# Kernel optimization log

Measured on AMD Instinct MI355X. Metric: run time of the kernel, lower is better.

## Reference

```python
import jax, jax.numpy as jnp
import numpy as np

B, DIM, L = 16, 512, 4096          # batch, hidden, num frames
N_FFT, HOP, WIN = 1024, 256, 1024  # STFT config (padding='same')


def setup_inputs() -> dict:
    key = jax.random.key(0)
    k1, k2, k3 = jax.random.split(key, 3)
    x = jax.random.normal(k1, (B, DIM, L), dtype=jnp.float32)
    # Conv1d(dim, 2*n_fft, kernel_size=1) weight/bias; small scale so exp(mag) stays sane
    W = jax.random.normal(k2, (2 * N_FFT, DIM), dtype=jnp.float32) * 0.02
    b = jax.random.normal(k3, (2 * N_FFT,), dtype=jnp.float32) * 0.02
    return {"x": x, "W": W, "b": b}


def reference(x, W, b):
    # 1x1 conv == channel-mixing GEMM: (B, 2*n_fft, L)
    h = jnp.einsum('bdl,od->bol', x, W) + b[None, :, None]
    mag, p = jnp.split(h, 2, axis=1)            # each (B, n_fft, L)
    mag = jnp.minimum(jnp.exp(mag), 100.0)      # exp then clip(max=100)
    S = mag * jax.lax.complex(jnp.cos(p), jnp.sin(p))
    # torch.fft.irfft(S, n_fft, dim=1): crops freq axis to n_fft//2+1 bins
    frames = jnp.fft.irfft(S, n=N_FFT, axis=1)
    # hann window, periodic=True (torch default)
    window = 0.5 * (1.0 - jnp.cos(2.0 * jnp.pi * jnp.arange(WIN, dtype=jnp.float32) / WIN))
    frames = frames * window[None, :, None]
    T = frames.shape[-1]
    out_len = (T - 1) * HOP + WIN
    idx = jnp.arange(T)[None, :] * HOP + jnp.arange(WIN)[:, None]
    y = jnp.zeros((frames.shape[0], out_len), frames.dtype).at[:, idx].add(frames)
    env = jnp.zeros((out_len,), frames.dtype).at[idx].add(
        jnp.broadcast_to((window * window)[:, None], (WIN, T)))
    pad = (WIN - HOP) // 2                      # 'same' padding trim
    return y[:, pad:out_len - pad] / env[pad:out_len - pad]
```

## Files before the change

### kernel.cpp

```cpp
#include <hip/hip_runtime.h>
#include <cstdint>
#include <cstddef>

#define BATCH  16
#define DIMK   512
#define LEN    4096
#define NFFT   1024
#define HOPS   256
#define PADT   384
#define OUTL   1048576
#define KP2    1056
#define KP2U   528
#define K2     4224

typedef __attribute__((ext_vector_type(8))) short  short8;
typedef __attribute__((ext_vector_type(4))) float  f32x4;

__device__ __forceinline__ unsigned short f2bf(float f) {
    unsigned u = __float_as_uint(f);
    u += 0x7FFFu + ((u >> 16) & 1u);
    return (unsigned short)(u >> 16);
}

__device__ __forceinline__ void gld16(const unsigned short* g, unsigned short* l) {
    __builtin_amdgcn_global_load_lds(
        (const __attribute__((address_space(1))) unsigned int*)(const void*)g,
        (__attribute__((address_space(3))) unsigned int*)(void*)l, 16, 0, 0);
}

__global__ void pack_W(const float* __restrict__ W, const float* __restrict__ bvec,
                       unsigned short* __restrict__ Wb, float* __restrict__ bp) {
    const int r = blockIdx.x;
    const int i = r >> 7, j = r & 127;
    const int src = (j < 64) ? (i * 64 + j) : (1024 + i * 64 + (j - 64));
    for (int c = threadIdx.x; c < DIMK; c += 256)
        Wb[r * DIMK + c] = f2bf(W[src * DIMK + c]);
    if (threadIdx.x == 0) bp[r] = bvec[src];
}

__global__ void transpose_x(const float* __restrict__ x, unsigned short* __restrict__ xT) {
    __shared__ float tile[32][33];
    const int b = blockIdx.z;
    const int l0 = blockIdx.x * 32, d0 = blockIdx.y * 32;
    const int tx = threadIdx.x, ty = threadIdx.y;
#pragma unroll
    for (int i = 0; i < 4; ++i)
        tile[ty + 8 * i][tx] = x[((size_t)b * DIMK + d0 + ty + 8 * i) * LEN + l0 + tx];
    __syncthreads();
#pragma unroll
    for (int i = 0; i < 4; ++i)
        xT[((size_t)b * LEN + l0 + ty + 8 * i) * DIMK + d0 + tx] = f2bf(tile[tx][ty + 8 * i]);
}

__global__ void build_D(unsigned short* __restrict__ D) {
    const int idx = blockIdx.x * 256 + threadIdx.x;
    if (idx >= 256 * K2) return;
    const int srow = idx / K2;
    const int col  = idx - srow * K2;
    const int rseg = col / KP2;
    const int jj   = col - rseg * KP2;
    const int n    = srow + 256 * rseg;
    const int k    = jj >> 1;
    const float wv = 0.5f - 0.5f * __cosf((float)n * (6.283185307179586f / 1024.f));
    float v = 0.f;
    if ((jj & 1) == 0) {
        if (k == 0)        v = wv * (1.f / 1024.f);
        else if (k < 512) {
            const int p = (k * n) & 1023;
            v = 2.f * __cosf((float)p * (6.283185307179586f / 1024.f)) * wv * (1.f / 1024.f);
        } else if (k == 512) v = ((n & 1) ? -wv : wv) * (1.f / 1024.f);
    } else {
        if (k >= 1 && k < 512) {
            const int p = (k * n) & 1023;
            v = -2.f * __sinf((float)p * (6.283185307179586f / 1024.f)) * wv * (1.f / 1024.f);
        }
    }
    D[idx] = f2bf(v);
}

__global__ __launch_bounds__(256)
void gemm1_kernel(const unsigned short* __restrict__ A,
                  const unsigned short* __restrict__ Bm,
                  const float* __restrict__ bp,
                  unsigned* __restrict__ Sout)
{
    __shared__ alignas(16) char smem[17408];
    unsigned short* Alds = (unsigned short*)smem;
    unsigned short* Blds = (unsigned short*)(smem + 8192);
    unsigned*       epi  = (unsigned*)smem;

    const int tid  = threadIdx.x;
    const int lane = tid & 63, w = tid >> 6;
    const int quad = lane >> 4, ln = lane & 15;
    const int bx = blockIdx.x, by = blockIdx.y, bz = blockIdx.z;
    const int l0 = bx * 128;

    const int c0 = tid, c1 = tid + 256;
    const unsigned short* Bsrc0 = Bm + ((size_t)bz * LEN + l0 + (c0 >> 2)) * DIMK + (c0 & 3) * 8;
    const unsigned short* Bsrc1 = Bm + ((size_t)bz * LEN + l0 + (c1 >> 2)) * DIMK + (c1 & 3) * 8;

    for (int mi = 0; mi < 3; ++mi) {
        const int mt = by * 3 + mi;
        const int m0 = mt * 128;
        const int kbase = mt * 64;

        const unsigned short* Asrc0 = A + (size_t)(m0 + (c0 >> 2)) * DIMK + (c0 & 3) * 8;
        const unsigned short* Asrc1 = A + (size_t)(m0 + (c1 >> 2)) * DIMK + (c1 & 3) * 8;

        f32x4 acc[8][2];
#pragma unroll
        for (int a = 0; a < 8; ++a)
#pragma unroll
            for (int c = 0; c < 2; ++c) acc[a][c] = (f32x4){0.f, 0.f, 0.f, 0.f};

        for (int k0 = 0; k0 < DIMK; k0 += 32) {
            gld16(Asrc0 + k0, &Alds[c0 * 8]);
            gld16(Asrc1 + k0, &Alds[c1 * 8]);
            gld16(Bsrc0 + k0, &Blds[c0 * 8]);
            gld16(Bsrc1 + k0, &Blds[c1 * 8]);
            __syncthreads();

            short8 af[8], bfr[2];
#pragma unroll
            for (int rt = 0; rt < 8; ++rt)
                af[rt] = *(const short8*)&Alds[((16 * rt + ln) * 4 + quad) * 8];
#pragma unroll
            for (int ct = 0; ct < 2; ++ct)
                bfr[ct] = *(const short8*)&Blds[((32 * w + 16 * ct + ln) * 4 + quad) * 8];
#pragma unroll
            for (int rt = 0; rt < 8; ++rt)
#pragma unroll
                for (int ct = 0; ct < 2; ++ct)
                    acc[rt][ct] = __builtin_amdgcn_mfma_f32_16x16x32_bf16(af[rt], bfr[ct], acc[rt][ct], 0, 0, 0);
            __syncthreads();
        }

#pragma unroll
        for (int ct = 0; ct < 2; ++ct) {
            const int lrow = w * 16 + ln;
#pragma unroll
            for (int rt = 0; rt < 4; ++rt) {
                unsigned pk[4];
#pragma unroll
                for (int reg = 0; reg < 4; ++reg) {
                    const int rloc = 16 * rt + quad * 4 + reg;
                    const float hm = acc[rt][ct][reg]     + bp[m0 + rloc];
                    const float hp = acc[rt + 4][ct][reg] + bp[m0 + 64 + rloc];
                    const float mag = fminf(__expf(hm), 100.0f);
                    pk[reg] = (unsigned)f2bf(mag * __cosf(hp)) |
                              ((unsigned)f2bf(mag * __sinf(hp)) << 16);
                }
                *(uint4*)&epi[lrow * 68 + 16 * rt + 4 * quad] = *(uint4*)pk;
            }
            __syncthreads();
#pragma unroll
            for (int i = 0; i < 4; ++i) {
                const int c = i * 256 + tid;
                const int row = c >> 4, kc = c & 15;
                if (kbase + kc * 4 < KP2U) {
                    const int l = l0 + 32 * (row >> 4) + 16 * ct + (row & 15);
                    uint4 v = *(const uint4*)&epi[row * 68 + kc * 4];
                    *(uint4*)&Sout[((size_t)bz * LEN + l) * KP2U + kbase + kc * 4] = v;
                }
            }
            __syncthreads();
        }
    }
}

__device__ __forceinline__ float env_at(int q, int s) {
    float env = 0.f;
#pragma unroll
    for (int r = 0; r < 4; ++r) {
        const int t = q - r;
        if (t >= 0 && t < LEN) {
            const float w = 0.5f - 0.5f * __cosf((float)(s + 256 * r) * (6.283185307179586f / 1024.f));
            env += w * w;
        }
    }
    return env;
}

__global__ __launch_bounds__(256)
void gemm2_kernel(const unsigned short* __restrict__ D,
                  const unsigned short* __restrict__ Sm,
                  float* __restrict__ yout)
{
    __shared__ alignas(16) char smem[24832];
    unsigned short* Albuf = (unsigned short*)smem;
    unsigned short* Blds  = (unsigned short*)(smem + 16384);
    float*          epi   = (float*)smem;

    const int tid  = threadIdx.x;
    const int lane = tid & 63, w = tid >> 6;
    const int quad = lane >> 4, ln = lane & 15;
    const int sh = w >> 1, qh = w & 1;
    const int bx = blockIdx.x, by = blockIdx.y, bz = blockIdx.z;
    const int qt0 = bx * 128, s0 = by * 128;

    const size_t srowbase = (size_t)bz * LEN;
    const int ca0 = tid, ca1 = tid + 256;

    f32x4 acc[4][4];
#pragma unroll
    for (int a = 0; a < 4; ++a)
#pragma unroll
        for (int c = 0; c < 4; ++c) acc[a][c] = (f32x4){0.f, 0.f, 0.f, 0.f};

    for (int kk = 0; kk < KP2; kk += 32) {
        {
            const int r0 = ca0 >> 2, q0 = ca0 & 3, le0 = qt0 + r0 - 2;
            const int r1 = ca1 >> 2, q1 = ca1 & 3, le1 = qt0 + r1 - 2;
            uint4 v0 = {0, 0, 0, 0}, v1 = {0, 0, 0, 0};
            if ((unsigned)le0 < (unsigned)LEN)
                v0 = *(const uint4*)&Sm[(srowbase + le0) * KP2 + kk + q0 * 8];
            if ((unsigned)le1 < (unsigned)LEN)
                v1 = *(const uint4*)&Sm[(srowbase + le1) * KP2 + kk + q1 * 8];
            *(uint4*)&Blds[ca0 * 8] = v0;
            *(uint4*)&Blds[ca1 * 8] = v1;
            if (tid < 16) {
                const int c2 = 512 + tid;
                const int r2 = c2 >> 2, q2 = c2 & 3, le2 = qt0 + r2 - 2;
                uint4 v2 = {0, 0, 0, 0};
                if ((unsigned)le2 < (unsigned)LEN)
                    v2 = *(const uint4*)&Sm[(srowbase + le2) * KP2 + kk + q2 * 8];
                *(uint4*)&Blds[c2 * 8] = v2;
            }
        }
        gld16(D + (size_t)(s0 + (ca0 >> 2)) * K2 + kk + (ca0 & 3) * 8, &Albuf[ca0 * 8]);
        gld16(D + (size_t)(s0 + (ca1 >> 2)) * K2 + kk + (ca1 & 3) * 8, &Albuf[ca1 * 8]);
        __syncthreads();

#pragma unroll
        for (int rseg = 0; rseg < 4; ++rseg) {
            const int buf = rseg & 1;
            if (rseg < 3) {
                const unsigned short* src = D + (rseg + 1) * KP2 + kk;
                gld16(src + (size_t)(s0 + (ca0 >> 2)) * K2 + (ca0 & 3) * 8,
                      &Albuf[(buf ^ 1) * 4096 + ca0 * 8]);
                gld16(src + (size_t)(s0 + (ca1 >> 2)) * K2 + (ca1 & 3) * 8,
                      &Albuf[(buf ^ 1) * 4096 + ca1 * 8]);
            }
            short8 af[4], bfr[4];
#pragma unroll
            for (int rt = 0; rt < 4; ++rt)
                af[rt] = *(const short8*)&Albuf[buf * 4096 + ((64 * sh + 16 * rt + ln) * 4 + quad) * 8];
#pragma unroll
            for (int ct = 0; ct < 4; ++ct)
                bfr[ct] = *(const short8*)&Blds[((3 - rseg + 64 * qh + 16 * ct + ln) * 4 + quad) * 8];
#pragma unroll
            for (int rt = 0; rt < 4; ++rt)
#pragma unroll
                for (int ct = 0; ct < 4; ++ct)
                    acc[rt][ct] = __builtin_amdgcn_mfma_f32_16x16x32_bf16(af[rt], bfr[ct], acc[rt][ct], 0, 0, 0);
            __syncthreads();
        }
    }

    float* yb = yout + (size_t)bz * OUTL;
#pragma unroll
    for (int ct = 0; ct < 4; ++ct) {
        const int qrow = qh * 16 + ln;
#pragma unroll
        for (int rt = 0; rt < 4; ++rt)
            *(f32x4*)&epi[qrow * 132 + 64 * sh + 16 * rt + 4 * quad] = acc[rt][ct];
        __syncthreads();
#pragma unroll
        for (int i = 0; i < 4; ++i) {
            const int c = i * 256 + tid;
            const int row = c >> 5, sc = c & 31;
            const int qi = qt0 + 64 * (row >> 4) + 16 * ct + (row & 15);
            const int q = qi + 1;
            const int j = 256 * qi + (s0 + sc * 4) - 128;
            if ((unsigned)j < (unsigned)(OUTL - 3)) {
                f32x4 v = *(const f32x4*)&epi[row * 132 + sc * 4];
                if (q >= 3 && q <= 4095) {
                    v *= (2.0f / 3.0f);
                } else {
#pragma unroll
                    for (int e = 0; e < 4; ++e)
                        v[e] /= env_at(q, s0 + sc * 4 + e);
                }
                *(f32x4*)&yb[j] = v;
            }
        }
        __syncthreads();
    }
}

extern "C" void kernel_launch(void* const* d_in, const int* in_sizes, int n_in,
                              void* d_out, int out_size, void* d_ws, size_t ws_size,
                              hipStream_t stream) {
    const float* x    = (const float*)d_in[0];
    const float* W    = (const float*)d_in[1];
    const float* bvec = (const float*)d_in[2];
    float* y = (float*)d_out;
    char* ws = (char*)d_ws;

    unsigned short* xT = (unsigned short*)(ws);
    unsigned short* Wb = (unsigned short*)(ws + 67108864);
    float*          bp = (float*)(ws + 68288512);
    unsigned short* D  = (unsigned short*)(ws + 68293120);
    unsigned*       S  = (unsigned*)(ws + 70455808);

    transpose_x<<<dim3(128, 16, BATCH), dim3(32, 8), 0, stream>>>(x, xT);
    pack_W<<<dim3(1152), dim3(256), 0, stream>>>(W, bvec, Wb, bp);
    build_D<<<dim3((256 * K2 + 255) / 256), dim3(256), 0, stream>>>(D);

    gemm1_kernel<<<dim3(32, 3, BATCH), dim3(256), 0, stream>>>(Wb, xT, bp, S);

    gemm2_kernel<<<dim3(33, 2, BATCH), dim3(256), 0, stream>>>(
        D, (const unsigned short*)S, y);
}
```

Measured before the change: 528.3 us.

## Restructure gemm2 main loop into per-wave A staging with double-buffered B

Each wave now stages its own A tile slice into a private LDS region through direct global-to-LDS loads. The B operand is double-buffered in LDS, with the next k-step's loads prefetched into registers. Block-wide barriers drop from five per k-step to one, replaced by vmcnt/lgkmcnt waits and sched barriers, so global loads overlap MFMA work. This doubles LDS use, which may lower occupancy, and the hand-set waitcnt counts are fragile.

```diff
diff --git a/kernel.cpp b/kernel.cpp
--- a/kernel.cpp
+++ b/kernel.cpp
@@ -20,6 +20,10 @@
     unsigned u = __float_as_uint(f);
     u += 0x7FFFu + ((u >> 16) & 1u);
     return (unsigned short)(u >> 16);
+}
+
+__device__ __forceinline__ int clampL(int v) {
+    return v < 0 ? 0 : (v > LEN - 1 ? LEN - 1 : v);
 }
 
 __device__ __forceinline__ void gld16(const unsigned short* g, unsigned short* l) {
@@ -186,10 +190,9 @@
                   const unsigned short* __restrict__ Sm,
                   float* __restrict__ yout)
 {
-    __shared__ alignas(16) char smem[24832];
-    unsigned short* Albuf = (unsigned short*)smem;
-    unsigned short* Blds  = (unsigned short*)(smem + 16384);
-    float*          epi   = (float*)smem;
+    __shared__ alignas(16) char smem[49664];
+    unsigned short* Bh  = (unsigned short*)(smem + 32768);
+    float*          epi = (float*)smem;
 
     const int tid  = threadIdx.x;
     const int lane = tid & 63, w = tid >> 6;
@@ -198,8 +201,34 @@
     const int bx = blockIdx.x, by = blockIdx.y, bz = blockIdx.z;
     const int qt0 = bx * 128, s0 = by * 128;
 
+    unsigned short* AW = (unsigned short*)smem + w * 4096;
+
     const size_t srowbase = (size_t)bz * LEN;
     const int ca0 = tid, ca1 = tid + 256;
+    const int c2  = 512 + (tid & 15);
+    const int c2w = 512 + tid;
+
+    const int le0 = qt0 + (ca0 >> 2) - 2;
+    const int le1 = qt0 + (ca1 >> 2) - 2;
+    const int le2 = qt0 + (c2  >> 2) - 2;
+    const size_t ba0 = (srowbase + (size_t)clampL(le0)) * KP2 + (ca0 & 3) * 8;
+    const size_t ba1 = (srowbase + (size_t)clampL(le1)) * KP2 + (ca1 & 3) * 8;
+    const size_t ba2 = (srowbase + (size_t)clampL(le2)) * KP2 + (c2  & 3) * 8;
+    const bool ok0 = (unsigned)le0 < (unsigned)LEN;
+    const bool ok1 = (unsigned)le1 < (unsigned)LEN;
+    const bool ok2 = (unsigned)le2 < (unsigned)LEN;
+    const uint4 zz = {0u, 0u, 0u, 0u};
+
+    const unsigned short* Dw = D + (size_t)(s0 + 64 * sh + (lane >> 2)) * K2 + (lane & 3) * 8;
+    unsigned short* ALn = AW + lane * 8;
+
+    auto stageA = [&](int kkel, int rseg, int buf) {
+        const unsigned short* p = Dw + rseg * KP2 + kkel;
+        unsigned short* l = ALn + buf * 2048;
+#pragma unroll
+        for (int j = 0; j < 4; ++j)
+            gld16(p + (size_t)(16 * j) * K2, l + j * 512);
+    };
 
     f32x4 acc[4][4];
 #pragma unroll
@@ -207,55 +236,89 @@
 #pragma unroll
         for (int c = 0; c < 4; ++c) acc[a][c] = (f32x4){0.f, 0.f, 0.f, 0.f};
 
-    for (int kk = 0; kk < KP2; kk += 32) {
-        {
-            const int r0 = ca0 >> 2, q0 = ca0 & 3, le0 = qt0 + r0 - 2;
-            const int r1 = ca1 >> 2, q1 = ca1 & 3, le1 = qt0 + r1 - 2;
-            uint4 v0 = {0, 0, 0, 0}, v1 = {0, 0, 0, 0};
-            if ((unsigned)le0 < (unsigned)LEN)
-                v0 = *(const uint4*)&Sm[(srowbase + le0) * KP2 + kk + q0 * 8];
-            if ((unsigned)le1 < (unsigned)LEN)
-                v1 = *(const uint4*)&Sm[(srowbase + le1) * KP2 + kk + q1 * 8];
-            *(uint4*)&Blds[ca0 * 8] = v0;
-            *(uint4*)&Blds[ca1 * 8] = v1;
-            if (tid < 16) {
-                const int c2 = 512 + tid;
-                const int r2 = c2 >> 2, q2 = c2 & 3, le2 = qt0 + r2 - 2;
-                uint4 v2 = {0, 0, 0, 0};
-                if ((unsigned)le2 < (unsigned)LEN)
-                    v2 = *(const uint4*)&Sm[(srowbase + le2) * KP2 + kk + q2 * 8];
-                *(uint4*)&Blds[c2 * 8] = v2;
-            }
-        }
-        gld16(D + (size_t)(s0 + (ca0 >> 2)) * K2 + kk + (ca0 & 3) * 8, &Albuf[ca0 * 8]);
-        gld16(D + (size_t)(s0 + (ca1 >> 2)) * K2 + kk + (ca1 & 3) * 8, &Albuf[ca1 * 8]);
-        __syncthreads();
-
-#pragma unroll
-        for (int rseg = 0; rseg < 4; ++rseg) {
-            const int buf = rseg & 1;
-            if (rseg < 3) {
-                const unsigned short* src = D + (rseg + 1) * KP2 + kk;
-                gld16(src + (size_t)(s0 + (ca0 >> 2)) * K2 + (ca0 & 3) * 8,
-                      &Albuf[(buf ^ 1) * 4096 + ca0 * 8]);
-                gld16(src + (size_t)(s0 + (ca1 >> 2)) * K2 + (ca1 & 3) * 8,
-                      &Albuf[(buf ^ 1) * 4096 + ca1 * 8]);
-            }
-            short8 af[4], bfr[4];
-#pragma unroll
-            for (int rt = 0; rt < 4; ++rt)
-                af[rt] = *(const short8*)&Albuf[buf * 4096 + ((64 * sh + 16 * rt + ln) * 4 + quad) * 8];
+    auto mfmaStep = [&](int rr, int buf, int h) {
+        short8 af[4], bfr[4];
+#pragma unroll
+        for (int rt = 0; rt < 4; ++rt)
+            af[rt] = *(const short8*)&AW[buf * 2048 + (16 * rt + ln) * 32 + quad * 8];
+#pragma unroll
+        for (int ct = 0; ct < 4; ++ct)
+            bfr[ct] = *(const short8*)&Bh[h * 4224 + ((3 - rr + 64 * qh + 16 * ct + ln) * 4 + quad) * 8];
+#pragma unroll
+        for (int rt = 0; rt < 4; ++rt)
 #pragma unroll
             for (int ct = 0; ct < 4; ++ct)
-                bfr[ct] = *(const short8*)&Blds[((3 - rseg + 64 * qh + 16 * ct + ln) * 4 + quad) * 8];
-#pragma unroll
-            for (int rt = 0; rt < 4; ++rt)
-#pragma unroll
-                for (int ct = 0; ct < 4; ++ct)
-                    acc[rt][ct] = __builtin_amdgcn_mfma_f32_16x16x32_bf16(af[rt], bfr[ct], acc[rt][ct], 0, 0, 0);
-            __syncthreads();
-        }
-    }
+                acc[rt][ct] = __builtin_amdgcn_mfma_f32_16x16x32_bf16(af[rt], bfr[ct], acc[rt][ct], 0, 0, 0);
+    };
+
+    uint4 v0, v1, v2;
+    auto loadB = [&](int kkel) {
+        v0 = *(const uint4*)&Sm[ba0 + kkel];
+        v1 = *(const uint4*)&Sm[ba1 + kkel];
+        v2 = *(const uint4*)&Sm[ba2 + kkel];
+        if (!ok0) v0 = zz;
+        if (!ok1) v1 = zz;
+        if (!ok2) v2 = zz;
+    };
+    auto writeB = [&](int h) {
+        unsigned short* Bp = Bh + h * 4224;
+        *(uint4*)&Bp[ca0 * 8] = v0;
+        *(uint4*)&Bp[ca1 * 8] = v1;
+        if (tid < 16) *(uint4*)&Bp[c2w * 8] = v2;
+    };
+
+#define WAITVM(NSTR)                                                        \
+    asm volatile("s_waitcnt vmcnt(" NSTR ")" ::: "memory");                 \
+    __builtin_amdgcn_sched_barrier(0);
+#define LGKM0                                                               \
+    asm volatile("s_waitcnt lgkmcnt(0)" ::: "memory");                      \
+    __builtin_amdgcn_sched_barrier(0);
+
+    loadB(0);
+    stageA(0, 0, 0);
+    stageA(0, 1, 1);
+    writeB(0);
+    LGKM0
+    __builtin_amdgcn_s_barrier();
+    __builtin_amdgcn_sched_barrier(0);
+
+    for (int kkIdx = 0; kkIdx < 33; ++kkIdx) {
+        const int kk  = kkIdx * 32;
+        const int kkn = (kkIdx < 32) ? kk + 32 : kk;
+        const int h   = kkIdx & 1;
+
+        loadB(kkn);
+        WAITVM("7")
+        mfmaStep(0, 0, h);
+        LGKM0
+        stageA(kk, 2, 0);
+        WAITVM("7")
+        mfmaStep(1, 1, h);
+        LGKM0
+        stageA(kk, 3, 1);
+        WAITVM("4")
+        asm volatile("" :: "v"(v0.x), "v"(v0.y), "v"(v0.z), "v"(v0.w),
+                           "v"(v1.x), "v"(v1.y), "v"(v1.z), "v"(v1.w),
+                           "v"(v2.x), "v"(v2.y), "v"(v2.z), "v"(v2.w));
+        mfmaStep(2, 0, h);
+        LGKM0
+        stageA(kkn, 0, 0);
+        WAITVM("4")
+        mfmaStep(3, 1, h);
+        LGKM0
+        stageA(kkn, 1, 1);
+        if (kkIdx != 32) {
+            writeB(h ^ 1);
+            LGKM0
+            __builtin_amdgcn_s_barrier();
+            __builtin_amdgcn_sched_barrier(0);
+        }
+    }
+#undef WAITVM
+#undef LGKM0
+
+    asm volatile("s_waitcnt vmcnt(0) lgkmcnt(0)" ::: "memory");
+    __syncthreads();
 
     float* yb = yout + (size_t)bz * OUTL;
 #pragma unroll
```

After: 565.9 us. 7.1% more time.
